# Optimization experiments

Measured on AMD Instinct MI355X. Metric: run time of the kernel, lower is better.

Reference implementation:

```python
import jax, jax.numpy as jnp
import numpy as np

H, LMAX, NSEG, EPS = 8, 2, 16, 1e-7
S = (LMAX + 1) ** 2  # 9 spherical components
L_OF_M = jnp.asarray(np.floor(np.sqrt(np.arange(S))).astype(np.int32))  # degree l of each m-component


def so3_linear(x, W, b):
    # x [n,S,Cin]; W [LMAX+1,Cin,Cout] per-degree weights; bias only on l=0 (invariant) component
    y = jnp.einsum('nsi,sio->nso', x, W[L_OF_M])
    return y + b[None, None, :] * (jnp.arange(S) == 0)[None, :, None]


def equiv_layernorm(x, gamma, beta):
    # x [N,S,C]; standard LN on l=0 scalars, RMS-of-irrep-norm scaling (equivariant) for l>0
    x0 = x[:, 0, :]
    mu = jnp.mean(x0, -1, keepdims=True)
    var = jnp.mean((x0 - mu) ** 2, -1, keepdims=True)
    outs = [(((x0 - mu) / jnp.sqrt(var + EPS)) * gamma[0] + beta)[:, None, :]]
    for l in range(1, LMAX + 1):
        xl = x[:, l * l:(l + 1) * (l + 1), :]               # [N,2l+1,C]
        n2 = jnp.mean(xl * xl, axis=1)                      # [N,C] mean sq over m
        rms = jnp.sqrt(jnp.mean(n2, -1, keepdims=True) + EPS)  # [N,1]
        outs.append(xl / rms[:, None, :] * gamma[l][None, None, :])
    return jnp.concatenate(outs, axis=1)


def setup_inputs() -> dict:
    key = jax.random.key(0)
    ks = jax.random.split(key, 12)
    N, E, CIN, CH = 512, 8192, 128, 256
    return dict(
        q=jax.random.normal(ks[0], (N, S, CIN), jnp.float32),
        k=jax.random.normal(ks[1], (N, S, CIN), jnp.float32),
        v=jax.random.normal(ks[2], (N, S, CIN), jnp.float32),
        envelope=jax.random.uniform(ks[3], (E,), jnp.float32),
        attn_bias=jax.random.normal(ks[4], (H, E), jnp.float32),
        atom_index=jax.random.randint(ks[5], (E,), 0, N),
        batch_index=jnp.sort(jax.random.randint(ks[6], (E,), 0, NSEG)),
        edge_map_tab=jax.random.randint(ks[7], (E,), 0, E),
        Wq=jax.random.normal(ks[8], (LMAX + 1, CIN, CH), jnp.float32) / np.float32(np.sqrt(CIN)),
        bq=jnp.zeros((CH,), jnp.float32),
        Wk=jax.random.normal(ks[9], (LMAX + 1, CIN, CH), jnp.float32) / np.float32(np.sqrt(CIN)),
        bk=jnp.zeros((CH,), jnp.float32),
        Wv=jax.random.normal(ks[10], (LMAX + 1, CIN, CH), jnp.float32) / np.float32(np.sqrt(CIN)),
        bv=jnp.zeros((CH,), jnp.float32),
        gamma=jnp.ones((LMAX + 1, CH), jnp.float32),
        beta=jnp.zeros((CH,), jnp.float32),
        Wo=jax.random.normal(ks[11], (LMAX + 1, CH, CIN), jnp.float32) / np.float32(np.sqrt(CH)),
        bo=jnp.zeros((CIN,), jnp.float32),
    )


def reference(q, k, v, envelope, attn_bias, atom_index, batch_index, edge_map_tab,
              Wq, bq, Wk, bk, Wv, bv, gamma, beta, Wo, bo):
    N, E = q.shape[0], atom_index.shape[0]
    qh = so3_linear(q, Wq, bq)                      # [N,S,CH]
    kh = so3_linear(k, Wk, bk)[atom_index]          # [E,S,CH] gather per edge
    vh = so3_linear(v, Wv, bv)[atom_index]
    CH = qh.shape[-1]
    d = CH // H
    qh = qh.reshape(N, S, H, d).transpose(2, 0, 1, 3).reshape(H, N, S * d)
    kh = kh.reshape(E, S, H, d).transpose(2, 0, 1, 3).reshape(H, E, S * d)
    vh = vh.reshape(E, S, H, d).transpose(2, 0, 1, 3).reshape(H, E, S * d)
    scale = np.float32(np.sqrt(d / 3.0) / d)
    scores = jnp.einsum('hnf,hef->hne', qh * scale, kh)         # [H,N,E]
    scores = scores + attn_bias[:, edge_map_tab][:, None, :]
    env_e = envelope[edge_map_tab]                               # [E]
    # smooth scatter softmax grouped by batch_index over edge axis
    st = scores.transpose(2, 0, 1)                               # [E,H,N]
    mx = jax.ops.segment_max(st, batch_index, num_segments=NSEG)
    rec = jnp.exp(st - mx[batch_index]) * env_e[:, None, None]
    den = jax.ops.segment_sum(rec, batch_index, num_segments=NSEG)
    attn = rec / (den[batch_index] + 1e-16)
    attn = (attn * env_e[:, None, None]).transpose(1, 2, 0)      # [H,N,E]
    out = jnp.einsum('hne,hef->hnf', attn, vh)                   # [H,N,S*d]
    out = out.transpose(1, 0, 2).reshape(N, H, S, d).transpose(0, 2, 1, 3).reshape(N, S, CH)
    out = equiv_layernorm(out, gamma, beta)
    return so3_linear(out, Wo, bo)
```

## Files before the change

### kernel.cpp

```cpp
#include <hip/hip_runtime.h>
#include <hip/hip_bf16.h>
#include <math.h>

#define NH 8
#define SDIM 9
#define NSEG 16
#define NATOM 512
#define NEDGE 8192
#define CIN 128
#define CHN 256
#define DH 32
#define FDIM 288
#define EPS 1e-7f
#define SCALE 0.10206207261596577f

typedef __attribute__((ext_vector_type(8))) short bf16x8;
typedef __attribute__((ext_vector_type(8))) short short8;
typedef __attribute__((ext_vector_type(4))) float f32x4;

__device__ inline float blockReduceMax(float v, float* red) {
    #pragma unroll
    for (int off = 32; off; off >>= 1) v = fmaxf(v, __shfl_xor(v, off, 64));
    int lane = threadIdx.x & 63, wid = threadIdx.x >> 6;
    if (lane == 0) red[wid] = v;
    __syncthreads();
    v = fmaxf(fmaxf(red[0], red[1]), fmaxf(red[2], red[3]));
    __syncthreads();
    return v;
}
__device__ inline float blockReduceSum(float v, float* red) {
    #pragma unroll
    for (int off = 32; off; off >>= 1) v += __shfl_xor(v, off, 64);
    int lane = threadIdx.x & 63, wid = threadIdx.x >> 6;
    if (lane == 0) red[wid] = v;
    __syncthreads();
    v = red[0] + red[1] + red[2] + red[3];
    __syncthreads();
    return v;
}
__device__ inline int lower_bound_batch(const int* __restrict__ b, int val) {
    int lo = 0, hi = NEDGE;
    while (lo < hi) {
        int mid = (lo + hi) >> 1;
        if (b[mid] < val) lo = mid + 1; else hi = mid;
    }
    return lo;
}
__device__ inline ushort f2bu(float x) {
    __hip_bfloat16 b = __float2bfloat16(x);
    return *(ushort*)&b;
}

__global__ void __launch_bounds__(256) stage1(const int* __restrict__ batch,
                                              const int* __restrict__ am, const int* __restrict__ emap,
                                              const float* __restrict__ envelope,
                                              const float* __restrict__ attn_bias,
                                              float* __restrict__ E1, float* __restrict__ E2,
                                              const float* __restrict__ q, const float* __restrict__ k,
                                              const float* __restrict__ v,
                                              const float* __restrict__ Wq, const float* __restrict__ Wk,
                                              const float* __restrict__ Wv,
                                              const float* __restrict__ bq, const float* __restrict__ bk,
                                              const float* __restrict__ bv,
                                              ushort* __restrict__ qhB,
                                              ushort* __restrict__ khB,
                                              ushort* __restrict__ vhT,
                                              const float* __restrict__ Wo,
                                              ushort* __restrict__ WoT) {
    const int bid = blockIdx.x;
    const int tid = threadIdx.x;
    if (bid < NSEG * NH) {
        const int seg = bid & (NSEG - 1), h = bid >> 4;
        __shared__ float e1[NATOM];
        __shared__ float e2[NATOM];
        __shared__ float red[4];
        e1[tid] = 0.f; e1[tid + 256] = 0.f;
        e2[tid] = 0.f; e2[tid + 256] = 0.f;
        const float* bh = attn_bias + (size_t)h * NEDGE;
        float mv = -1e30f;
        for (int e = tid; e < NEDGE; e += 256) mv = fmaxf(mv, bh[e]);
        const float mb = blockReduceMax(mv, red);
        const int st = lower_bound_batch(batch, seg);
        const int en = lower_bound_batch(batch, seg + 1);
        for (int e = st + tid; e < en; e += 256) {
            int m = am[e], em = emap[e];
            float ev = envelope[em];
            float eb = __expf(bh[em] - mb);
            atomicAdd(&e1[m], ev * eb);
            atomicAdd(&e2[m], ev * ev * eb);
        }
        __syncthreads();
        size_t base = ((size_t)h * NSEG + seg) * NATOM;
        E1[base + tid] = e1[tid]; E1[base + tid + 256] = e1[tid + 256];
        E2[base + tid] = e2[tid]; E2[base + tid + 256] = e2[tid + 256];
        return;
    }
    if (bid < NSEG * NH + 48) {
        const int t = bid - NSEG * NH;
        const int l = t / 16;
        const int cb = (t & 15) >> 2, ob = t & 3;
        const int c0 = cb * 64, o0 = ob * 32;
        __shared__ float tile[64][33];
        const float* src = Wo + (size_t)l * CHN * CIN;
        #pragma unroll
        for (int p = 0; p < 8; ++p) {
            int row = p * 8 + (tid >> 5);
            int col = tid & 31;
            tile[row][col] = src[(size_t)(c0 + row) * CIN + o0 + col];
        }
        __syncthreads();
        ushort* dst = WoT + (size_t)l * CIN * CHN;
        #pragma unroll
        for (int p = 0; p < 8; ++p) {
            int o = p * 4 + (tid >> 6);
            int c = tid & 63;
            dst[(size_t)(o0 + o) * CHN + c0 + c] = f2bu(tile[c][o]);
        }
        return;
    }
    {
        const int idx = bid - (NSEG * NH + 48);
        const int z = idx / 144;
        const int rem = idx - z * 144;
        const int s = rem >> 4;
        const int n0 = (rem & 15) * 32;
        const int l = (s == 0) ? 0 : ((s < 4) ? 1 : 2);
        const float* x = (z == 0) ? q : (z == 1) ? k : v;
        const float* W = ((z == 0) ? Wq : (z == 1) ? Wk : Wv) + (size_t)l * CIN * CHN;
        const float* bias = (z == 0) ? bq : (z == 1) ? bk : bv;
        const int lane = tid & 63, w = tid >> 6;
        const int wr = w >> 1, wc = w & 1;
        const int r = lane & 15, kg = lane >> 4;
        const int arow = n0 + 16 * wr + r;
        const float* xrow = x + ((size_t)arow * SDIM + s) * CIN;
        f32x4 acc[8] = {};
        #pragma unroll
        for (int ks = 0; ks < 4; ++ks) {
            const int k0 = ks * 32 + kg * 8;
            float4 x0 = *(const float4*)(xrow + k0);
            float4 x1 = *(const float4*)(xrow + k0 + 4);
            bf16x8 a;
            a[0] = f2bu(x0.x); a[1] = f2bu(x0.y); a[2] = f2bu(x0.z); a[3] = f2bu(x0.w);
            a[4] = f2bu(x1.x); a[5] = f2bu(x1.y); a[6] = f2bu(x1.z); a[7] = f2bu(x1.w);
            #pragma unroll
            for (int j = 0; j < 8; ++j) {
                const int o = 128 * wc + 16 * j + r;
                const float* wp = W + (size_t)k0 * CHN + o;
                bf16x8 bf;
                #pragma unroll
                for (int jj = 0; jj < 8; ++jj) bf[jj] = f2bu(wp[(size_t)jj * CHN]);
                acc[j] = __builtin_amdgcn_mfma_f32_16x16x32_bf16(a, bf, acc[j], 0, 0, 0);
            }
        }
        const float sc = (z == 0) ? SCALE : 1.0f;
        #pragma unroll
        for (int j = 0; j < 8; ++j) {
            const int o = 128 * wc + 16 * j + r;
            const float bb = (s == 0) ? bias[o] : 0.f;
            const int h = o >> 5, dj = o & 31;
            const int f = s * DH + dj;
            if (z < 2) {
                ushort* dst = (z == 0) ? qhB : khB;
                #pragma unroll
                for (int p = 0; p < 4; ++p) {
                    int row = n0 + 16 * wr + kg * 4 + p;
                    dst[((size_t)h * NATOM + row) * FDIM + f] = f2bu((acc[j][p] + bb) * sc);
                }
            } else {
                ushort* dst = vhT + ((size_t)h * FDIM + f) * NATOM;
                #pragma unroll
                for (int p = 0; p < 4; ++p) {
                    int row = n0 + 16 * wr + kg * 4 + p;
                    dst[row] = f2bu(acc[j][p] + bb);
                }
            }
        }
    }
}

__global__ void __launch_bounds__(256) gemm_scores_mfma(const ushort* __restrict__ qhB,
                                                        const ushort* __restrict__ khB,
                                                        float* __restrict__ scoresA) {
    const int h = blockIdx.z;
    const int m0 = blockIdx.x * 64;
    const int n0 = blockIdx.y * 64;
    const int tid = threadIdx.x;
    const int lane = tid & 63, w = tid >> 6;
    const int wr = w >> 1, wc = w & 1;
    const int r = lane & 15, kg = lane >> 4;
    const ushort* A = qhB + (size_t)h * NATOM * FDIM;
    const ushort* B = khB + (size_t)h * NATOM * FDIM;
    const int ar = n0 + 32 * wr + r;
    const int br = m0 + 32 * wc + r;
    f32x4 acc00 = {}, acc01 = {}, acc10 = {}, acc11 = {};
    #pragma unroll
    for (int ks = 0; ks < FDIM / 32; ++ks) {
        const int k0 = ks * 32 + kg * 8;
        bf16x8 a0 = *(const bf16x8*)(A + (size_t)ar * FDIM + k0);
        bf16x8 a1 = *(const bf16x8*)(A + (size_t)(ar + 16) * FDIM + k0);
        bf16x8 b0 = *(const bf16x8*)(B + (size_t)br * FDIM + k0);
        bf16x8 b1 = *(const bf16x8*)(B + (size_t)(br + 16) * FDIM + k0);
        acc00 = __builtin_amdgcn_mfma_f32_16x16x32_bf16(a0, b0, acc00, 0, 0, 0);
        acc01 = __builtin_amdgcn_mfma_f32_16x16x32_bf16(a0, b1, acc01, 0, 0, 0);
        acc10 = __builtin_amdgcn_mfma_f32_16x16x32_bf16(a1, b0, acc10, 0, 0, 0);
        acc11 = __builtin_amdgcn_mfma_f32_16x16x32_bf16(a1, b1, acc11, 0, 0, 0);
    }
    #define STORE_SC(ACC, I, J) { \
        int row = n0 + 32 * wr + (I) * 16 + kg * 4; \
        int col = m0 + 32 * wc + (J) * 16 + r; \
        float* dst = scoresA + ((size_t)h * NATOM + row) * NATOM + col; \
        dst[0] = ACC[0]; dst[NATOM] = ACC[1]; dst[2 * NATOM] = ACC[2]; dst[3 * NATOM] = ACC[3]; }
    STORE_SC(acc00, 0, 0) STORE_SC(acc01, 0, 1) STORE_SC(acc10, 1, 0) STORE_SC(acc11, 1, 1)
    #undef STORE_SC
}

#define SMW_RPW 4
__global__ void __launch_bounds__(256) softmax_agg3(const float* __restrict__ scoresA,
                                                    ushort* __restrict__ attnB,
                                                    const float* __restrict__ E1,
                                                    const float* __restrict__ E2) {
    const int h = blockIdx.y;
    const int n0 = blockIdx.x * (4 * SMW_RPW);
    __shared__ float E1s[NSEG][NATOM];
    __shared__ float E2s[NSEG][NATOM];
    const int tid = threadIdx.x;
    const float* e1g = E1 + (size_t)h * NSEG * NATOM;
    const float* e2g = E2 + (size_t)h * NSEG * NATOM;
    for (int i = tid * 4; i < NSEG * NATOM; i += 1024) {
        *(float4*)&((float*)E1s)[i] = *(const float4*)&e1g[i];
        *(float4*)&((float*)E2s)[i] = *(const float4*)&e2g[i];
    }
    __syncthreads();
    const int lane = tid & 63, wid = tid >> 6;
    const int m0 = lane * 8;
    for (int rr = 0; rr < SMW_RPW; ++rr) {
        const int row = n0 + wid * SMW_RPW + rr;
        const float* srow = scoresA + ((size_t)h * NATOM + row) * NATOM;
        float4 sa = *(const float4*)(srow + m0);
        float4 sb = *(const float4*)(srow + m0 + 4);
        float s[8] = {sa.x, sa.y, sa.z, sa.w, sb.x, sb.y, sb.z, sb.w};
        float mx = fmaxf(fmaxf(fmaxf(s[0], s[1]), fmaxf(s[2], s[3])),
                         fmaxf(fmaxf(s[4], s[5]), fmaxf(s[6], s[7])));
        #pragma unroll
        for (int off = 32; off; off >>= 1) mx = fmaxf(mx, __shfl_xor(mx, off, 64));
        float es[8];
        #pragma unroll
        for (int j = 0; j < 8; ++j) es[j] = __expf(s[j] - mx);
        float D[NSEG];
        #pragma unroll
        for (int g = 0; g < NSEG; ++g) {
            float4 p = *(const float4*)&E1s[g][m0];
            float4 p2 = *(const float4*)&E1s[g][m0 + 4];
            D[g] = es[0] * p.x + es[1] * p.y + es[2] * p.z + es[3] * p.w
                 + es[4] * p2.x + es[5] * p2.y + es[6] * p2.z + es[7] * p2.w;
        }
        #pragma unroll
        for (int g = 0; g < NSEG; ++g) {
            float vv = D[g];
            #pragma unroll
            for (int off = 32; off; off >>= 1) vv += __shfl_xor(vv, off, 64);
            D[g] = vv;
        }
        float w[8] = {};
        #pragma unroll
        for (int g = 0; g < NSEG; ++g) {
            float iv = 1.0f / (D[g] + 1e-30f);
            float4 p = *(const float4*)&E2s[g][m0];
            float4 p2 = *(const float4*)&E2s[g][m0 + 4];
            w[0] += iv * p.x;  w[1] += iv * p.y;  w[2] += iv * p.z;  w[3] += iv * p.w;
            w[4] += iv * p2.x; w[5] += iv * p2.y; w[6] += iv * p2.z; w[7] += iv * p2.w;
        }
        ushort* arow = attnB + ((size_t)h * NATOM + row) * NATOM;
        short8 ov;
        #pragma unroll
        for (int j = 0; j < 8; ++j) ov[j] = (short)f2bu(es[j] * w[j]);
        *(short8*)(arow + m0) = ov;
    }
}

__global__ void __launch_bounds__(256) gemm_out_mfma(const ushort* __restrict__ attnB,
                                                     const ushort* __restrict__ vhT,
                                                     float* __restrict__ attnOut) {
    const int h = blockIdx.z;
    const int f0 = blockIdx.x * 64;
    const int n0 = blockIdx.y * 64;
    const int tid = threadIdx.x;
    const int lane = tid & 63, w = tid >> 6;
    const int wr = w >> 1, wc = w & 1;
    const int r = lane & 15, kg = lane >> 4;
    const ushort* A = attnB + (size_t)h * NATOM * NATOM;
    const ushort* B = vhT + (size_t)h * FDIM * NATOM;
    const int ar = n0 + 32 * wr + r;
    const int br = f0 + 32 * wc + r;
    const bool b0ok = (f0 + 32 * wc) < FDIM;
    const bool b1ok = (f0 + 32 * wc + 16) < FDIM;
    f32x4 acc00 = {}, acc01 = {}, acc10 = {}, acc11 = {};
    const bf16x8 bz = {};
    #pragma unroll 4
    for (int ks = 0; ks < NATOM / 32; ++ks) {
        const int k0 = ks * 32 + kg * 8;
        bf16x8 a0 = *(const bf16x8*)(A + (size_t)ar * NATOM + k0);
        bf16x8 a1 = *(const bf16x8*)(A + (size_t)(ar + 16) * NATOM + k0);
        bf16x8 b0 = b0ok ? *(const bf16x8*)(B + (size_t)br * NATOM + k0) : bz;
        bf16x8 b1 = b1ok ? *(const bf16x8*)(B + (size_t)(br + 16) * NATOM + k0) : bz;
        acc00 = __builtin_amdgcn_mfma_f32_16x16x32_bf16(a0, b0, acc00, 0, 0, 0);
        acc01 = __builtin_amdgcn_mfma_f32_16x16x32_bf16(a0, b1, acc01, 0, 0, 0);
        acc10 = __builtin_amdgcn_mfma_f32_16x16x32_bf16(a1, b0, acc10, 0, 0, 0);
        acc11 = __builtin_amdgcn_mfma_f32_16x16x32_bf16(a1, b1, acc11, 0, 0, 0);
    }
    #define STORE_OUT(ACC, I, J) { \
        int row = n0 + 32 * wr + (I) * 16 + kg * 4; \
        int f = f0 + 32 * wc + (J) * 16 + r; \
        if (f < FDIM) { \
            int s = f >> 5, dj = f & 31; \
            float* dst = attnOut + ((size_t)row * SDIM + s) * CHN + h * DH + dj; \
            dst[0] = ACC[0]; dst[SDIM * CHN] = ACC[1]; dst[2 * SDIM * CHN] = ACC[2]; dst[3 * SDIM * CHN] = ACC[3]; } }
    STORE_OUT(acc00, 0, 0) STORE_OUT(acc01, 0, 1) STORE_OUT(acc10, 1, 0) STORE_OUT(acc11, 1, 1)
    #undef STORE_OUT
}

__global__ void __launch_bounds__(256) eqln_bf16(const float* __restrict__ xin,
                                                 const float* __restrict__ gamma,
                                                 const float* __restrict__ beta,
                                                 ushort* __restrict__ outn) {
    const int n = blockIdx.x;
    const int c = threadIdx.x;
    __shared__ float red[4];
    float xv[SDIM];
    #pragma unroll
    for (int s = 0; s < SDIM; ++s) xv[s] = xin[((size_t)n * SDIM + s) * CHN + c];
    float mu = blockReduceSum(xv[0], red) * (1.0f / CHN);
    float dv = xv[0] - mu;
    float var = blockReduceSum(dv * dv, red) * (1.0f / CHN);
    float y0 = dv / sqrtf(var + EPS) * gamma[c] + beta[c];
    outn[(size_t)n * SDIM * CHN + c] = f2bu(y0);
    float n2 = (xv[1] * xv[1] + xv[2] * xv[2] + xv[3] * xv[3]) * (1.0f / 3.0f);
    float ms = blockReduceSum(n2, red) * (1.0f / CHN);
    float inv1 = 1.0f / sqrtf(ms + EPS);
    #pragma unroll
    for (int s = 1; s < 4; ++s)
        outn[((size_t)n * SDIM + s) * CHN + c] = f2bu(xv[s] * inv1 * gamma[CHN + c]);
    float n22 = (xv[4] * xv[4] + xv[5] * xv[5] + xv[6] * xv[6] + xv[7] * xv[7] + xv[8] * xv[8]) * (1.0f / 5.0f);
    float ms2 = blockReduceSum(n22, red) * (1.0f / CHN);
    float inv2 = 1.0f / sqrtf(ms2 + EPS);
    #pragma unroll
    for (int s = 4; s < SDIM; ++s)
        outn[((size_t)n * SDIM + s) * CHN + c] = f2bu(xv[s] * inv2 * gamma[2 * CHN + c]);
}

__global__ void __launch_bounds__(256) so3out_mfma(const ushort* __restrict__ normedB,
                                                   const ushort* __restrict__ WoT,
                                                   const float* __restrict__ bo,
                                                   float* __restrict__ out) {
    const int s = blockIdx.y;
    const int n0 = blockIdx.x * 64;
    const int l = (s == 0) ? 0 : ((s < 4) ? 1 : 2);
    const int tid = threadIdx.x;
    const int lane = tid & 63, w = tid >> 6;
    const int wr = w >> 1, wc = w & 1;
    const int r = lane & 15, kg = lane >> 4;
    const ushort* B = WoT + (size_t)l * CIN * CHN;
    const int ar = n0 + 32 * wr + r;
    const int bc = 64 * wc;
    f32x4 acc[2][4] = {};
    #pragma unroll
    for (int ks = 0; ks < CHN / 32; ++ks) {
        const int k0 = ks * 32 + kg * 8;
        bf16x8 a0 = *(const bf16x8*)(normedB + ((size_t)ar * SDIM + s) * CHN + k0);
        bf16x8 a1 = *(const bf16x8*)(normedB + ((size_t)(ar + 16) * SDIM + s) * CHN + k0);
        bf16x8 b[4];
        #pragma unroll
        for (int j = 0; j < 4; ++j)
            b[j] = *(const bf16x8*)(B + (size_t)(bc + 16 * j + r) * CHN + k0);
        #pragma unroll
        for (int j = 0; j < 4; ++j) {
            acc[0][j] = __builtin_amdgcn_mfma_f32_16x16x32_bf16(a0, b[j], acc[0][j], 0, 0, 0);
            acc[1][j] = __builtin_amdgcn_mfma_f32_16x16x32_bf16(a1, b[j], acc[1][j], 0, 0, 0);
        }
    }
    #pragma unroll
    for (int i = 0; i < 2; ++i) {
        #pragma unroll
        for (int j = 0; j < 4; ++j) {
            int n = n0 + 32 * wr + 16 * i + kg * 4;
            int o = bc + 16 * j + r;
            float badd = (s == 0) ? bo[o] : 0.f;
            float* dst = out + ((size_t)n * SDIM + s) * CIN + o;
            dst[0] = acc[i][j][0] + badd;
            dst[SDIM * CIN] = acc[i][j][1] + badd;
            dst[2 * SDIM * CIN] = acc[i][j][2] + badd;
            dst[3 * SDIM * CIN] = acc[i][j][3] + badd;
        }
    }
}

extern "C" void kernel_launch(void* const* d_in, const int* in_sizes, int n_in,
                              void* d_out, int out_size, void* d_ws, size_t ws_size,
                              hipStream_t stream) {
    const float* q = (const float*)d_in[0];
    const float* k = (const float*)d_in[1];
    const float* v = (const float*)d_in[2];
    const float* envelope = (const float*)d_in[3];
    const float* attn_bias = (const float*)d_in[4];
    const int* atom_index = (const int*)d_in[5];
    const int* batch_index = (const int*)d_in[6];
    const int* edge_map = (const int*)d_in[7];
    const float* Wq = (const float*)d_in[8];
    const float* bq = (const float*)d_in[9];
    const float* Wk = (const float*)d_in[10];
    const float* bk = (const float*)d_in[11];
    const float* Wv = (const float*)d_in[12];
    const float* bv = (const float*)d_in[13];
    const float* gamma = (const float*)d_in[14];
    const float* beta = (const float*)d_in[15];
    const float* Wo = (const float*)d_in[16];
    const float* bo = (const float*)d_in[17];
    float* out = (float*)d_out;

    const size_t SZ_HNF = (size_t)NH * NATOM * FDIM;
    const size_t SZ_HNN = (size_t)NH * NATOM * NATOM;
    const size_t SZ_TAB = (size_t)NH * NSEG * NATOM;
    const size_t SZ_WOT = (size_t)3 * CIN * CHN;

    char* wsb = (char*)d_ws;
    ushort* qhB = (ushort*)wsb;
    ushort* khB = qhB + SZ_HNF;
    ushort* vhT = khB + SZ_HNF;
    float* scoresA = (float*)(vhT + SZ_HNF);
    ushort* attnB = (ushort*)(scoresA + SZ_HNN);
    float* E1 = (float*)(attnB + SZ_HNN);
    float* E2 = E1 + SZ_TAB;
    ushort* WoT = (ushort*)(E2 + SZ_TAB);
    float* attnOut = scoresA;
    ushort* normedB = qhB;

    size_t needed = 2 * 3 * SZ_HNF + 4 * SZ_HNN + 2 * SZ_HNN + 4 * 2 * SZ_TAB + 2 * SZ_WOT + 256;
    if (ws_size < needed) return;

    stage1<<<NSEG * NH + 48 + 432, 256, 0, stream>>>(
        batch_index, atom_index, edge_map, envelope, attn_bias, E1, E2,
        q, k, v, Wq, Wk, Wv, bq, bk, bv, qhB, khB, vhT, Wo, WoT);
    gemm_scores_mfma<<<dim3(NATOM / 64, NATOM / 64, NH), 256, 0, stream>>>(qhB, khB, scoresA);
    softmax_agg3<<<dim3(NATOM / (4 * SMW_RPW), NH), 256, 0, stream>>>(scoresA, attnB, E1, E2);
    gemm_out_mfma<<<dim3((FDIM + 63) / 64, NATOM / 64, NH), 256, 0, stream>>>(attnB, vhT, attnOut);
    eqln_bf16<<<NATOM, 256, 0, stream>>>(attnOut, gamma, beta, normedB);
    so3out_mfma<<<dim3(NATOM / 64, SDIM), 256, 0, stream>>>(normedB, WoT, bo, out);
}
```

Baseline: 78.13 us.

## Fuse scores GEMM with softmax, and fold layernorm stats into output GEMMs

Merges the QK score GEMM with the segment softmax so the fp32 score matrix is never written to or read back from global memory. The PV GEMM now accumulates per-row layernorm statistics with atomics into a buffer zeroed in stage1. The final SO3 linear applies the normalization while loading its input, which removes the separate layernorm kernel. This cuts two kernel launches and a large intermediate round trip, at the cost of atomic contention, a var=E[x^2]-mu^2 formulation that is less numerically stable, and a fused kernel with smaller tiles and more redundant K loads.

```diff
diff --git a/kernel.cpp b/kernel.cpp
--- a/kernel.cpp
+++ b/kernel.cpp
@@ -25,16 +25,6 @@
     if (lane == 0) red[wid] = v;
     __syncthreads();
     v = fmaxf(fmaxf(red[0], red[1]), fmaxf(red[2], red[3]));
-    __syncthreads();
-    return v;
-}
-__device__ inline float blockReduceSum(float v, float* red) {
-    #pragma unroll
-    for (int off = 32; off; off >>= 1) v += __shfl_xor(v, off, 64);
-    int lane = threadIdx.x & 63, wid = threadIdx.x >> 6;
-    if (lane == 0) red[wid] = v;
-    __syncthreads();
-    v = red[0] + red[1] + red[2] + red[3];
     __syncthreads();
     return v;
 }
@@ -66,7 +56,8 @@
                                               ushort* __restrict__ khB,
                                               ushort* __restrict__ vhT,
                                               const float* __restrict__ Wo,
-                                              ushort* __restrict__ WoT) {
+                                              ushort* __restrict__ WoT,
+                                              float* __restrict__ stats) {
     const int bid = blockIdx.x;
     const int tid = threadIdx.x;
     if (bid < NSEG * NH) {
@@ -118,7 +109,7 @@
         }
         return;
     }
-    {
+    if (bid < NSEG * NH + 48 + 432) {
         const int idx = bid - (NSEG * NH + 48);
         const int z = idx / 144;
         const int rem = idx - z * 144;
@@ -175,221 +166,267 @@
                 }
             }
         }
-    }
-}
-
-__global__ void __launch_bounds__(256) gemm_scores_mfma(const ushort* __restrict__ qhB,
-                                                        const ushort* __restrict__ khB,
-                                                        float* __restrict__ scoresA) {
+        return;
+    }
+    {
+        float4 z4 = {0.f, 0.f, 0.f, 0.f};
+        float4* sp = (float4*)stats;
+        sp[tid] = z4;
+        sp[tid + 256] = z4;
+    }
+}
+
+__global__ void __launch_bounds__(256) attn_fused(const ushort* __restrict__ qhB,
+                                                  const ushort* __restrict__ khB,
+                                                  const float* __restrict__ E1,
+                                                  const float* __restrict__ E2,
+                                                  ushort* __restrict__ attnB) {
+    const int h = blockIdx.y;
+    const int n0 = blockIdx.x * 16;
+    __shared__ float E1s[NSEG][NATOM];
+    __shared__ float E2s[NSEG][NATOM];
+    __shared__ float rowmax[4][16];
+    __shared__ float Dpart[4][16][NSEG];
+    __shared__ float invDs[16][NSEG];
+    const int tid = threadIdx.x;
+    const int lane = tid & 63, w = tid >> 6;
+    const int r = lane & 15, kg = lane >> 4;
+    {
+        const float* e1g = E1 + (size_t)h * NSEG * NATOM;
+        const float* e2g = E2 + (size_t)h * NSEG * NATOM;
+        for (int i = tid * 4; i < NSEG * NATOM; i += 1024) {
+            *(float4*)&((float*)E1s)[i] = *(const float4*)&e1g[i];
+            *(float4*)&((float*)E2s)[i] = *(const float4*)&e2g[i];
+        }
+    }
+    const ushort* A = qhB + (size_t)h * NATOM * FDIM;
+    const ushort* B = khB + (size_t)h * NATOM * FDIM;
+    const int ar = n0 + r;
+    f32x4 acc[8] = {};
+    #pragma unroll
+    for (int ks = 0; ks < FDIM / 32; ++ks) {
+        const int k0 = ks * 32 + kg * 8;
+        bf16x8 a = *(const bf16x8*)(A + (size_t)ar * FDIM + k0);
+        #pragma unroll
+        for (int j = 0; j < 8; ++j) {
+            const int bcol = w * 128 + 16 * j + r;
+            bf16x8 b = *(const bf16x8*)(B + (size_t)bcol * FDIM + k0);
+            acc[j] = __builtin_amdgcn_mfma_f32_16x16x32_bf16(a, b, acc[j], 0, 0, 0);
+        }
+    }
+    __syncthreads();
+    float pm[4];
+    #pragma unroll
+    for (int p = 0; p < 4; ++p) {
+        float m = acc[0][p];
+        #pragma unroll
+        for (int j = 1; j < 8; ++j) m = fmaxf(m, acc[j][p]);
+        pm[p] = m;
+    }
+    #pragma unroll
+    for (int mk = 1; mk < 16; mk <<= 1)
+        #pragma unroll
+        for (int p = 0; p < 4; ++p) pm[p] = fmaxf(pm[p], __shfl_xor(pm[p], mk, 64));
+    if (r == 0) {
+        #pragma unroll
+        for (int p = 0; p < 4; ++p) rowmax[w][kg * 4 + p] = pm[p];
+    }
+    __syncthreads();
+    float mx[4];
+    #pragma unroll
+    for (int p = 0; p < 4; ++p) {
+        int row = kg * 4 + p;
+        mx[p] = fmaxf(fmaxf(rowmax[0][row], rowmax[1][row]),
+                      fmaxf(rowmax[2][row], rowmax[3][row]));
+    }
+    float es[8][4];
+    #pragma unroll
+    for (int j = 0; j < 8; ++j)
+        #pragma unroll
+        for (int p = 0; p < 4; ++p) es[j][p] = __expf(acc[j][p] - mx[p]);
+    float Dp[4][NSEG] = {};
+    #pragma unroll
+    for (int j = 0; j < 8; ++j) {
+        const int col = w * 128 + 16 * j + r;
+        #pragma unroll
+        for (int g = 0; g < NSEG; ++g) {
+            float e1 = E1s[g][col];
+            #pragma unroll
+            for (int p = 0; p < 4; ++p) Dp[p][g] += es[j][p] * e1;
+        }
+    }
+    #pragma unroll
+    for (int mk = 1; mk < 16; mk <<= 1)
+        #pragma unroll
+        for (int p = 0; p < 4; ++p)
+            #pragma unroll
+            for (int g = 0; g < NSEG; ++g) Dp[p][g] += __shfl_xor(Dp[p][g], mk, 64);
+    if (r == 0) {
+        #pragma unroll
+        for (int p = 0; p < 4; ++p)
+            #pragma unroll
+            for (int g = 0; g < NSEG; ++g) Dpart[w][kg * 4 + p][g] = Dp[p][g];
+    }
+    __syncthreads();
+    {
+        int row = tid >> 4, g = tid & 15;
+        float d = Dpart[0][row][g] + Dpart[1][row][g] + Dpart[2][row][g] + Dpart[3][row][g];
+        invDs[row][g] = 1.0f / (d + 1e-30f);
+    }
+    __syncthreads();
+    float iv[4][NSEG];
+    #pragma unroll
+    for (int p = 0; p < 4; ++p)
+        #pragma unroll
+        for (int g = 0; g < NSEG; ++g) iv[p][g] = invDs[kg * 4 + p][g];
+    ushort* sbuf = (ushort*)E1s;
+    #pragma unroll
+    for (int j = 0; j < 8; ++j) {
+        const int col = w * 128 + 16 * j + r;
+        float ww[4] = {};
+        #pragma unroll
+        for (int g = 0; g < NSEG; ++g) {
+            float e2 = E2s[g][col];
+            #pragma unroll
+            for (int p = 0; p < 4; ++p) ww[p] += e2 * iv[p][g];
+        }
+        #pragma unroll
+        for (int p = 0; p < 4; ++p)
+            sbuf[(kg * 4 + p) * NATOM + col] = f2bu(es[j][p] * ww[p]);
+    }
+    __syncthreads();
+    {
+        ushort* dst = attnB + ((size_t)h * NATOM + n0) * NATOM;
+        for (int i = tid * 8; i < 16 * NATOM; i += 2048)
+            *(short8*)(dst + i) = *(short8*)(sbuf + i);
+    }
+}
+
+__global__ void __launch_bounds__(256) gemm_out_stats(const ushort* __restrict__ attnB,
+                                                      const ushort* __restrict__ vhT,
+                                                      float* __restrict__ attnOut,
+                                                      float* __restrict__ stats) {
     const int h = blockIdx.z;
-    const int m0 = blockIdx.x * 64;
+    const int fb = blockIdx.x;
     const int n0 = blockIdx.y * 64;
     const int tid = threadIdx.x;
     const int lane = tid & 63, w = tid >> 6;
-    const int wr = w >> 1, wc = w & 1;
-    const int r = lane & 15, kg = lane >> 4;
-    const ushort* A = qhB + (size_t)h * NATOM * FDIM;
-    const ushort* B = khB + (size_t)h * NATOM * FDIM;
-    const int ar = n0 + 32 * wr + r;
-    const int br = m0 + 32 * wc + r;
-    f32x4 acc00 = {}, acc01 = {}, acc10 = {}, acc11 = {};
-    #pragma unroll
-    for (int ks = 0; ks < FDIM / 32; ++ks) {
-        const int k0 = ks * 32 + kg * 8;
-        bf16x8 a0 = *(const bf16x8*)(A + (size_t)ar * FDIM + k0);
-        bf16x8 a1 = *(const bf16x8*)(A + (size_t)(ar + 16) * FDIM + k0);
-        bf16x8 b0 = *(const bf16x8*)(B + (size_t)br * FDIM + k0);
-        bf16x8 b1 = *(const bf16x8*)(B + (size_t)(br + 16) * FDIM + k0);
-        acc00 = __builtin_amdgcn_mfma_f32_16x16x32_bf16(a0, b0, acc00, 0, 0, 0);
-        acc01 = __builtin_amdgcn_mfma_f32_16x16x32_bf16(a0, b1, acc01, 0, 0, 0);
-        acc10 = __builtin_amdgcn_mfma_f32_16x16x32_bf16(a1, b0, acc10, 0, 0, 0);
-        acc11 = __builtin_amdgcn_mfma_f32_16x16x32_bf16(a1, b1, acc11, 0, 0, 0);
-    }
-    #define STORE_SC(ACC, I, J) { \
-        int row = n0 + 32 * wr + (I) * 16 + kg * 4; \
-        int col = m0 + 32 * wc + (J) * 16 + r; \
-        float* dst = scoresA + ((size_t)h * NATOM + row) * NATOM + col; \
-        dst[0] = ACC[0]; dst[NATOM] = ACC[1]; dst[2 * NATOM] = ACC[2]; dst[3 * NATOM] = ACC[3]; }
-    STORE_SC(acc00, 0, 0) STORE_SC(acc01, 0, 1) STORE_SC(acc10, 1, 0) STORE_SC(acc11, 1, 1)
-    #undef STORE_SC
-}
-
-#define SMW_RPW 4
-__global__ void __launch_bounds__(256) softmax_agg3(const float* __restrict__ scoresA,
-                                                    ushort* __restrict__ attnB,
-                                                    const float* __restrict__ E1,
-                                                    const float* __restrict__ E2) {
-    const int h = blockIdx.y;
-    const int n0 = blockIdx.x * (4 * SMW_RPW);
-    __shared__ float E1s[NSEG][NATOM];
-    __shared__ float E2s[NSEG][NATOM];
-    const int tid = threadIdx.x;
-    const float* e1g = E1 + (size_t)h * NSEG * NATOM;
-    const float* e2g = E2 + (size_t)h * NSEG * NATOM;
-    for (int i = tid * 4; i < NSEG * NATOM; i += 1024) {
-        *(float4*)&((float*)E1s)[i] = *(const float4*)&e1g[i];
-        *(float4*)&((float*)E2s)[i] = *(const float4*)&e2g[i];
-    }
-    __syncthreads();
-    const int lane = tid & 63, wid = tid >> 6;
-    const int m0 = lane * 8;
-    for (int rr = 0; rr < SMW_RPW; ++rr) {
-        const int row = n0 + wid * SMW_RPW + rr;
-        const float* srow = scoresA + ((size_t)h * NATOM + row) * NATOM;
-        float4 sa = *(const float4*)(srow + m0);
-        float4 sb = *(const float4*)(srow + m0 + 4);
-        float s[8] = {sa.x, sa.y, sa.z, sa.w, sb.x, sb.y, sb.z, sb.w};
-        float mx = fmaxf(fmaxf(fmaxf(s[0], s[1]), fmaxf(s[2], s[3])),
-                         fmaxf(fmaxf(s[4], s[5]), fmaxf(s[6], s[7])));
-        #pragma unroll
-        for (int off = 32; off; off >>= 1) mx = fmaxf(mx, __shfl_xor(mx, off, 64));
-        float es[8];
-        #pragma unroll
-        for (int j = 0; j < 8; ++j) es[j] = __expf(s[j] - mx);
-        float D[NSEG];
-        #pragma unroll
-        for (int g = 0; g < NSEG; ++g) {
-            float4 p = *(const float4*)&E1s[g][m0];
-            float4 p2 = *(const float4*)&E1s[g][m0 + 4];
-            D[g] = es[0] * p.x + es[1] * p.y + es[2] * p.z + es[3] * p.w
-                 + es[4] * p2.x + es[5] * p2.y + es[6] * p2.z + es[7] * p2.w;
-        }
-        #pragma unroll
-        for (int g = 0; g < NSEG; ++g) {
-            float vv = D[g];
-            #pragma unroll
-            for (int off = 32; off; off >>= 1) vv += __shfl_xor(vv, off, 64);
-            D[g] = vv;
-        }
-        float w[8] = {};
-        #pragma unroll
-        for (int g = 0; g < NSEG; ++g) {
-            float iv = 1.0f / (D[g] + 1e-30f);
-            float4 p = *(const float4*)&E2s[g][m0];
-            float4 p2 = *(const float4*)&E2s[g][m0 + 4];
-            w[0] += iv * p.x;  w[1] += iv * p.y;  w[2] += iv * p.z;  w[3] += iv * p.w;
-            w[4] += iv * p2.x; w[5] += iv * p2.y; w[6] += iv * p2.z; w[7] += iv * p2.w;
-        }
-        ushort* arow = attnB + ((size_t)h * NATOM + row) * NATOM;
-        short8 ov;
-        #pragma unroll
-        for (int j = 0; j < 8; ++j) ov[j] = (short)f2bu(es[j] * w[j]);
-        *(short8*)(arow + m0) = ov;
-    }
-}
-
-__global__ void __launch_bounds__(256) gemm_out_mfma(const ushort* __restrict__ attnB,
-                                                     const ushort* __restrict__ vhT,
-                                                     float* __restrict__ attnOut) {
-    const int h = blockIdx.z;
-    const int f0 = blockIdx.x * 64;
-    const int n0 = blockIdx.y * 64;
-    const int tid = threadIdx.x;
-    const int lane = tid & 63, w = tid >> 6;
-    const int wr = w >> 1, wc = w & 1;
     const int r = lane & 15, kg = lane >> 4;
     const ushort* A = attnB + (size_t)h * NATOM * NATOM;
     const ushort* B = vhT + (size_t)h * FDIM * NATOM;
-    const int ar = n0 + 32 * wr + r;
-    const int br = f0 + 32 * wc + r;
-    const bool b0ok = (f0 + 32 * wc) < FDIM;
-    const bool b1ok = (f0 + 32 * wc + 16) < FDIM;
-    f32x4 acc00 = {}, acc01 = {}, acc10 = {}, acc11 = {};
-    const bf16x8 bz = {};
+    const int ar = n0 + 16 * w + r;
+    f32x4 acc[2] = {};
     #pragma unroll 4
     for (int ks = 0; ks < NATOM / 32; ++ks) {
         const int k0 = ks * 32 + kg * 8;
-        bf16x8 a0 = *(const bf16x8*)(A + (size_t)ar * NATOM + k0);
-        bf16x8 a1 = *(const bf16x8*)(A + (size_t)(ar + 16) * NATOM + k0);
-        bf16x8 b0 = b0ok ? *(const bf16x8*)(B + (size_t)br * NATOM + k0) : bz;
-        bf16x8 b1 = b1ok ? *(const bf16x8*)(B + (size_t)(br + 16) * NATOM + k0) : bz;
-        acc00 = __builtin_amdgcn_mfma_f32_16x16x32_bf16(a0, b0, acc00, 0, 0, 0);
-        acc01 = __builtin_amdgcn_mfma_f32_16x16x32_bf16(a0, b1, acc01, 0, 0, 0);
-        acc10 = __builtin_amdgcn_mfma_f32_16x16x32_bf16(a1, b0, acc10, 0, 0, 0);
-        acc11 = __builtin_amdgcn_mfma_f32_16x16x32_bf16(a1, b1, acc11, 0, 0, 0);
-    }
-    #define STORE_OUT(ACC, I, J) { \
-        int row = n0 + 32 * wr + (I) * 16 + kg * 4; \
-        int f = f0 + 32 * wc + (J) * 16 + r; \
-        if (f < FDIM) { \
-            int s = f >> 5, dj = f & 31; \
-            float* dst = attnOut + ((size_t)row * SDIM + s) * CHN + h * DH + dj; \
-            dst[0] = ACC[0]; dst[SDIM * CHN] = ACC[1]; dst[2 * SDIM * CHN] = ACC[2]; dst[3 * SDIM * CHN] = ACC[3]; } }
-    STORE_OUT(acc00, 0, 0) STORE_OUT(acc01, 0, 1) STORE_OUT(acc10, 1, 0) STORE_OUT(acc11, 1, 1)
-    #undef STORE_OUT
-}
-
-__global__ void __launch_bounds__(256) eqln_bf16(const float* __restrict__ xin,
+        bf16x8 a = *(const bf16x8*)(A + (size_t)ar * NATOM + k0);
+        bf16x8 b0 = *(const bf16x8*)(B + (size_t)(32 * fb + 16 * 0 + r) * NATOM + k0);
+        bf16x8 b1 = *(const bf16x8*)(B + (size_t)(32 * fb + 16 * 1 + r) * NATOM + k0);
+        acc[0] = __builtin_amdgcn_mfma_f32_16x16x32_bf16(a, b0, acc[0], 0, 0, 0);
+        acc[1] = __builtin_amdgcn_mfma_f32_16x16x32_bf16(a, b1, acc[1], 0, 0, 0);
+    }
+    float sA[4], sB[4];
+    #pragma unroll
+    for (int p = 0; p < 4; ++p) { sA[p] = 0.f; sB[p] = 0.f; }
+    #pragma unroll
+    for (int j = 0; j < 2; ++j) {
+        const int dj = 16 * j + r;
+        #pragma unroll
+        for (int p = 0; p < 4; ++p) {
+            const int row = n0 + 16 * w + kg * 4 + p;
+            float x = acc[j][p];
+            attnOut[((size_t)row * SDIM + fb) * CHN + h * DH + dj] = x;
+            sA[p] += x;
+            sB[p] += x * x;
+        }
+    }
+    #pragma unroll
+    for (int mk = 1; mk < 16; mk <<= 1)
+        #pragma unroll
+        for (int p = 0; p < 4; ++p) {
+            sA[p] += __shfl_xor(sA[p], mk, 64);
+            sB[p] += __shfl_xor(sB[p], mk, 64);
+        }
+    if (r == 0) {
+        #pragma unroll
+        for (int p = 0; p < 4; ++p) {
+            const int row = n0 + 16 * w + kg * 4 + p;
+            if (fb == 0) {
+                atomicAdd(&stats[row * 4 + 0], sA[p]);
+                atomicAdd(&stats[row * 4 + 1], sB[p]);
+            } else if (fb < 4) {
+                atomicAdd(&stats[row * 4 + 2], sB[p]);
+            } else {
+                atomicAdd(&stats[row * 4 + 3], sB[p]);
+            }
+        }
+    }
+}
+
+__global__ void __launch_bounds__(256) so3out_ln(const float* __restrict__ attnOut,
+                                                 const float* __restrict__ stats,
                                                  const float* __restrict__ gamma,
                                                  const float* __restrict__ beta,
-                                                 ushort* __restrict__ outn) {
-    const int n = blockIdx.x;
-    const int c = threadIdx.x;
-    __shared__ float red[4];
-    float xv[SDIM];
-    #pragma unroll
-    for (int s = 0; s < SDIM; ++s) xv[s] = xin[((size_t)n * SDIM + s) * CHN + c];
-    float mu = blockReduceSum(xv[0], red) * (1.0f / CHN);
-    float dv = xv[0] - mu;
-    float var = blockReduceSum(dv * dv, red) * (1.0f / CHN);
-    float y0 = dv / sqrtf(var + EPS) * gamma[c] + beta[c];
-    outn[(size_t)n * SDIM * CHN + c] = f2bu(y0);
-    float n2 = (xv[1] * xv[1] + xv[2] * xv[2] + xv[3] * xv[3]) * (1.0f / 3.0f);
-    float ms = blockReduceSum(n2, red) * (1.0f / CHN);
-    float inv1 = 1.0f / sqrtf(ms + EPS);
-    #pragma unroll
-    for (int s = 1; s < 4; ++s)
-        outn[((size_t)n * SDIM + s) * CHN + c] = f2bu(xv[s] * inv1 * gamma[CHN + c]);
-    float n22 = (xv[4] * xv[4] + xv[5] * xv[5] + xv[6] * xv[6] + xv[7] * xv[7] + xv[8] * xv[8]) * (1.0f / 5.0f);
-    float ms2 = blockReduceSum(n22, red) * (1.0f / CHN);
-    float inv2 = 1.0f / sqrtf(ms2 + EPS);
-    #pragma unroll
-    for (int s = 4; s < SDIM; ++s)
-        outn[((size_t)n * SDIM + s) * CHN + c] = f2bu(xv[s] * inv2 * gamma[2 * CHN + c]);
-}
-
-__global__ void __launch_bounds__(256) so3out_mfma(const ushort* __restrict__ normedB,
-                                                   const ushort* __restrict__ WoT,
-                                                   const float* __restrict__ bo,
-                                                   float* __restrict__ out) {
+                                                 const ushort* __restrict__ WoT,
+                                                 const float* __restrict__ bo,
+                                                 float* __restrict__ out) {
     const int s = blockIdx.y;
-    const int n0 = blockIdx.x * 64;
+    const int n0 = blockIdx.x * 16;
     const int l = (s == 0) ? 0 : ((s < 4) ? 1 : 2);
     const int tid = threadIdx.x;
     const int lane = tid & 63, w = tid >> 6;
-    const int wr = w >> 1, wc = w & 1;
     const int r = lane & 15, kg = lane >> 4;
+    const int ar = n0 + r;
+    float mu, ivl;
+    {
+        float s0 = stats[ar * 4 + 0];
+        float q0 = stats[ar * 4 + 1];
+        float q1 = stats[ar * 4 + 2];
+        float q2 = stats[ar * 4 + 3];
+        float m0 = s0 * (1.0f / CHN);
+        float var = q0 * (1.0f / CHN) - m0 * m0;
+        if (s == 0) { mu = m0; ivl = 1.0f / sqrtf(var + EPS); }
+        else if (s < 4) { mu = 0.f; ivl = 1.0f / sqrtf(q1 * (1.0f / (3 * CHN)) + EPS); }
+        else { mu = 0.f; ivl = 1.0f / sqrtf(q2 * (1.0f / (5 * CHN)) + EPS); }
+    }
+    const float* xrow = attnOut + ((size_t)ar * SDIM + s) * CHN;
+    const float* gl = gamma + l * CHN;
     const ushort* B = WoT + (size_t)l * CIN * CHN;
-    const int ar = n0 + 32 * wr + r;
-    const int bc = 64 * wc;
-    f32x4 acc[2][4] = {};
+    f32x4 acc[2] = {};
     #pragma unroll
     for (int ks = 0; ks < CHN / 32; ++ks) {
         const int k0 = ks * 32 + kg * 8;
-        bf16x8 a0 = *(const bf16x8*)(normedB + ((size_t)ar * SDIM + s) * CHN + k0);
-        bf16x8 a1 = *(const bf16x8*)(normedB + ((size_t)(ar + 16) * SDIM + s) * CHN + k0);
-        bf16x8 b[4];
-        #pragma unroll
-        for (int j = 0; j < 4; ++j)
-            b[j] = *(const bf16x8*)(B + (size_t)(bc + 16 * j + r) * CHN + k0);
-        #pragma unroll
-        for (int j = 0; j < 4; ++j) {
-            acc[0][j] = __builtin_amdgcn_mfma_f32_16x16x32_bf16(a0, b[j], acc[0][j], 0, 0, 0);
-            acc[1][j] = __builtin_amdgcn_mfma_f32_16x16x32_bf16(a1, b[j], acc[1][j], 0, 0, 0);
-        }
-    }
-    #pragma unroll
-    for (int i = 0; i < 2; ++i) {
-        #pragma unroll
-        for (int j = 0; j < 4; ++j) {
-            int n = n0 + 32 * wr + 16 * i + kg * 4;
-            int o = bc + 16 * j + r;
-            float badd = (s == 0) ? bo[o] : 0.f;
-            float* dst = out + ((size_t)n * SDIM + s) * CIN + o;
-            dst[0] = acc[i][j][0] + badd;
-            dst[SDIM * CIN] = acc[i][j][1] + badd;
-            dst[2 * SDIM * CIN] = acc[i][j][2] + badd;
-            dst[3 * SDIM * CIN] = acc[i][j][3] + badd;
+        float4 x0 = *(const float4*)(xrow + k0);
+        float4 x1 = *(const float4*)(xrow + k0 + 4);
+        float4 g0 = *(const float4*)(gl + k0);
+        float4 g1 = *(const float4*)(gl + k0 + 4);
+        float y[8];
+        y[0] = (x0.x - mu) * ivl * g0.x; y[1] = (x0.y - mu) * ivl * g0.y;
+        y[2] = (x0.z - mu) * ivl * g0.z; y[3] = (x0.w - mu) * ivl * g0.w;
+        y[4] = (x1.x - mu) * ivl * g1.x; y[5] = (x1.y - mu) * ivl * g1.y;
+        y[6] = (x1.z - mu) * ivl * g1.z; y[7] = (x1.w - mu) * ivl * g1.w;
+        if (s == 0) {
+            float4 b0 = *(const float4*)(beta + k0);
+            float4 b1 = *(const float4*)(beta + k0 + 4);
+            y[0] += b0.x; y[1] += b0.y; y[2] += b0.z; y[3] += b0.w;
+            y[4] += b1.x; y[5] += b1.y; y[6] += b1.z; y[7] += b1.w;
+        }
+        bf16x8 a;
+        #pragma unroll
+        for (int jj = 0; jj < 8; ++jj) a[jj] = f2bu(y[jj]);
+        bf16x8 b0f = *(const bf16x8*)(B + (size_t)(32 * w + 16 * 0 + r) * CHN + k0);
+        bf16x8 b1f = *(const bf16x8*)(B + (size_t)(32 * w + 16 * 1 + r) * CHN + k0);
+        acc[0] = __builtin_amdgcn_mfma_f32_16x16x32_bf16(a, b0f, acc[0], 0, 0, 0);
+        acc[1] = __builtin_amdgcn_mfma_f32_16x16x32_bf16(a, b1f, acc[1], 0, 0, 0);
+    }
+    #pragma unroll
+    for (int j = 0; j < 2; ++j) {
+        const int o = 32 * w + 16 * j + r;
+        const float badd = (s == 0) ? bo[o] : 0.f;
+        #pragma unroll
+        for (int p = 0; p < 4; ++p) {
+            const int n = n0 + kg * 4 + p;
+            out[((size_t)n * SDIM + s) * CIN + o] = acc[j][p] + badd;
         }
     }
 }
@@ -421,28 +458,27 @@
     const size_t SZ_HNN = (size_t)NH * NATOM * NATOM;
     const size_t SZ_TAB = (size_t)NH * NSEG * NATOM;
     const size_t SZ_WOT = (size_t)3 * CIN * CHN;
+    const size_t SZ_NSC = (size_t)NATOM * SDIM * CHN;
 
     char* wsb = (char*)d_ws;
     ushort* qhB = (ushort*)wsb;
     ushort* khB = qhB + SZ_HNF;
     ushort* vhT = khB + SZ_HNF;
-    float* scoresA = (float*)(vhT + SZ_HNF);
-    ushort* attnB = (ushort*)(scoresA + SZ_HNN);
-    float* E1 = (float*)(attnB + SZ_HNN);
+    ushort* attnB = vhT + SZ_HNF;
+    float* attnOut = (float*)(attnB + SZ_HNN);
+    float* E1 = attnOut + SZ_NSC;
     float* E2 = E1 + SZ_TAB;
     ushort* WoT = (ushort*)(E2 + SZ_TAB);
-    float* attnOut = scoresA;
-    ushort* normedB = qhB;
-
-    size_t needed = 2 * 3 * SZ_HNF + 4 * SZ_HNN + 2 * SZ_HNN + 4 * 2 * SZ_TAB + 2 * SZ_WOT + 256;
+    float* stats = (float*)(WoT + SZ_WOT);
+
+    size_t needed = 2 * 3 * SZ_HNF + 2 * SZ_HNN + 4 * SZ_NSC + 4 * 2 * SZ_TAB
+                  + 2 * SZ_WOT + 4 * NATOM * 4 + 256;
     if (ws_size < needed) return;
 
-    stage1<<<NSEG * NH + 48 + 432, 256, 0, stream>>>(
+    stage1<<<NSEG * NH + 48 + 432 + 1, 256, 0, stream>>>(
         batch_index, atom_index, edge_map, envelope, attn_bias, E1, E2,
-        q, k, v, Wq, Wk, Wv, bq, bk, bv, qhB, khB, vhT, Wo, WoT);
-    gemm_scores_mfma<<<dim3(NATOM / 64, NATOM / 64, NH), 256, 0, stream>>>(qhB, khB, scoresA);
-    softmax_agg3<<<dim3(NATOM / (4 * SMW_RPW), NH), 256, 0, stream>>>(scoresA, attnB, E1, E2);
-    gemm_out_mfma<<<dim3((FDIM + 63) / 64, NATOM / 64, NH), 256, 0, stream>>>(attnB, vhT, attnOut);
-    eqln_bf16<<<NATOM, 256, 0, stream>>>(attnOut, gamma, beta, normedB);
-    so3out_mfma<<<dim3(NATOM / 64, SDIM), 256, 0, stream>>>(normedB, WoT, bo, out);
-}
+        q, k, v, Wq, Wk, Wv, bq, bk, bv, qhB, khB, vhT, Wo, WoT, stats);
+    attn_fused<<<dim3(NATOM / 16, NH), 256, 0, stream>>>(qhB, khB, E1, E2, attnB);
+    gemm_out_stats<<<dim3(SDIM, NATOM / 64, NH), 256, 0, stream>>>(attnB, vhT, attnOut, stats);
+    so3out_ln<<<dim3(NATOM / 16, SDIM), 256, 0, stream>>>(attnOut, stats, gamma, beta, WoT, bo, out);
+}
```

Result: faster. 74.72 us (-4.4%).
